# Optimization experiments

Hardware: AMD Instinct MI355X
Metric: run time of the kernel (lower is better)

## Reference

```python
import jax, jax.numpy as jnp
import numpy as np
from jax import lax

N, E, G = 20000, 640000, 16
NA, H, NG, L, NC = 21, 128, 50, 6, 97
CUTOFF = 10.0
LOG2 = 0.6931471805599453

def ssp(v):
    # ShiftedSoftplus: softplus(x) - log(2)
    return jax.nn.softplus(v) - LOG2

def setup_inputs() -> dict:
    key = jax.random.key(0)
    ks = jax.random.split(key, 24)
    s = 0.08  # xavier-ish scale for 128-wide layers
    inp = {
        "x": jax.random.normal(ks[0], (N, NA), dtype=jnp.float32),
        "pos": jax.random.uniform(ks[1], (N, 3), dtype=jnp.float32, minval=0.0, maxval=30.0),
        "edge_index": jax.random.randint(ks[2], (2, E), 0, N, dtype=jnp.int64),
        "batch": jnp.sort(jax.random.randint(ks[3], (N,), 0, G, dtype=jnp.int64)),
        # embedding Linear(21 -> 128), weights stored [in, out]
        "emb_w": jax.random.normal(ks[4], (NA, H), dtype=jnp.float32) * 0.15,
        "emb_b": jnp.zeros((H,), dtype=jnp.float32),
        # per-interaction-block params, stacked over L layers
        "mlp1_w": jax.random.normal(ks[5], (L, NG, H), dtype=jnp.float32) * 0.12,
        "mlp1_b": jnp.zeros((L, H), dtype=jnp.float32),
        "mlp2_w": jax.random.normal(ks[6], (L, H, H), dtype=jnp.float32) * s,
        "mlp2_b": jnp.zeros((L, H), dtype=jnp.float32),
        "conv1_w": jax.random.normal(ks[7], (L, H, H), dtype=jnp.float32) * s,  # no bias
        "conv2_w": jax.random.normal(ks[8], (L, H, H), dtype=jnp.float32) * s,
        "conv2_b": jnp.zeros((L, H), dtype=jnp.float32),
        "lin_w": jax.random.normal(ks[9], (L, H, H), dtype=jnp.float32) * s,
        "lin_b": jnp.zeros((L, H), dtype=jnp.float32),
        # head (note: original reuses self.lin1 twice, act is ReLU, dropout eval=identity)
        "lin1_w": jax.random.normal(ks[10], (H, H), dtype=jnp.float32) * s,
        "lin1_b": jnp.zeros((H,), dtype=jnp.float32),
        "lin2_w": jax.random.normal(ks[11], (H, NC), dtype=jnp.float32) * s,
        "lin2_b": jnp.zeros((NC,), dtype=jnp.float32),
    }
    return inp

def reference(x, pos, edge_index, batch, emb_w, emb_b, mlp1_w, mlp1_b, mlp2_w,
              mlp2_b, conv1_w, conv2_w, conv2_b, lin_w, lin_b, lin1_w, lin1_b,
              lin2_w, lin2_b):
    row, col = edge_index[0], edge_index[1]  # source j, target i
    d = pos[row] - pos[col]                  # [E,3]
    edge_weight = jnp.sqrt(jnp.sum(d * d, axis=-1))  # [E]
    # Gaussian smearing
    offset = jnp.linspace(0.0, CUTOFF, NG)
    coeff = -0.5 / (offset[1] - offset[0]) ** 2
    edge_attr = jnp.exp(coeff * (edge_weight[:, None] - offset[None, :]) ** 2)  # [E,NG]
    # cosine cutoff
    C = 0.5 * (jnp.cos(edge_weight * jnp.pi / CUTOFF) + 1.0)  # [E]

    h = x @ emb_w + emb_b  # [N,H]

    def block(h, p):
        m1w, m1b, m2w, m2b, c1w, c2w, c2b, lw, lb = p
        # edge MLP filter times cutoff envelope
        Wf = (ssp(edge_attr @ m1w + m1b) @ m2w + m2b) * C[:, None]  # [E,H]
        hx = h @ c1w                                 # lin1 (no bias)
        msg = hx[row] * Wf                           # gather + modulate
        agg = jax.ops.segment_sum(msg, col, num_segments=N)  # scatter-add
        y = ssp(agg @ c2w + c2b)
        y = y @ lw + lb
        return h + y, None

    h, _ = lax.scan(block, h, (mlp1_w, mlp1_b, mlp2_w, mlp2_b,
                               conv1_w, conv2_w, conv2_b, lin_w, lin_b))

    h = jax.nn.relu(h @ lin1_w + lin1_b)
    # global mean pool
    ones = jnp.ones((N,), dtype=h.dtype)
    counts = jnp.maximum(jax.ops.segment_sum(ones, batch, num_segments=G), 1.0)
    graph_emb = jax.ops.segment_sum(h, batch, num_segments=G) / counts[:, None]  # [G,H]
    h2 = jax.nn.relu(graph_emb @ lin1_w + lin1_b)  # lin1 reused; dropout=identity (eval)
    out = h2 @ lin2_w + lin2_b                     # [G,NC]
    return graph_emb, out
```

## Files before the change

kernel.cpp:

```cpp
#include <hip/hip_runtime.h>
#include <hip/hip_bf16.h>

#define HD 128
#define NGAUSS 50
#define NLAYER 6
#define NGRAPH 16
#define NCLS 97
#define NTAB2 8192
#define WMAX 12.0f

typedef __attribute__((ext_vector_type(8))) short bf16x8;
typedef __attribute__((ext_vector_type(4))) float f32x4;
typedef __attribute__((ext_vector_type(8))) ushort u16x8;
typedef __attribute__((ext_vector_type(4))) ushort u16x4;

__device__ __forceinline__ float ssp_f(float x) {
    float e = __expf(-fabsf(x));
    return fmaxf(x, 0.0f) + __logf(0.5f + 0.5f * e);
}
__device__ __forceinline__ ushort f2bf(float f) {
    uint u = __float_as_uint(f);
    return (ushort)((u + 0x7FFFu + ((u >> 16) & 1u)) >> 16);
}
__device__ __forceinline__ float bf2f(ushort s) {
    return __uint_as_float(((uint)s) << 16);
}

__global__ void hist_kernel(const int* __restrict__ col, int* __restrict__ deg, int E) {
    int e = blockIdx.x * blockDim.x + threadIdx.x;
    if (e < E) atomicAdd(&deg[col[e]], 1);
}

__global__ void scan1_kernel(const int* __restrict__ deg, int* __restrict__ rowp,
                             int* __restrict__ bsum, int N) {
    __shared__ int sm[256];
    const int t = threadIdx.x, i = blockIdx.x * 256 + t;
    int v = (i < N) ? deg[i] : 0;
    sm[t] = v;
    __syncthreads();
    for (int off = 1; off < 256; off <<= 1) {
        int x = sm[t];
        int a = (t >= off) ? sm[t - off] : 0;
        __syncthreads();
        sm[t] = x + a;
        __syncthreads();
    }
    if (i < N) rowp[i] = sm[t] - v;
    if (t == 255) bsum[blockIdx.x] = sm[255];
}
__global__ void scan2_kernel(const int* __restrict__ bsum, int* __restrict__ boff,
                             int NB, int* __restrict__ rowpN) {
    __shared__ int sm[256];
    const int t = threadIdx.x;
    int v = (t < NB) ? bsum[t] : 0;
    sm[t] = v;
    __syncthreads();
    for (int off = 1; off < 256; off <<= 1) {
        int x = sm[t];
        int a = (t >= off) ? sm[t - off] : 0;
        __syncthreads();
        sm[t] = x + a;
        __syncthreads();
    }
    if (t < NB) boff[t] = sm[t] - v;
    if (t == 255) *rowpN = sm[255];
}
__global__ void scan3_kernel(int* __restrict__ rowp, const int* __restrict__ boff,
                             int* __restrict__ cursor, int N) {
    int i = blockIdx.x * blockDim.x + threadIdx.x;
    if (i < N) {
        int r = rowp[i] + boff[i >> 8];
        rowp[i] = r;
        cursor[i] = r;
    }
}

__global__ void fill_kernel(const int* __restrict__ row, const int* __restrict__ col,
                            const float* __restrict__ pos, int* __restrict__ cursor,
                            uint* __restrict__ meta, int E) {
    int e = blockIdx.x * blockDim.x + threadIdx.x;
    if (e >= E) return;
    int c = col[e], r = row[e];
    int slot = atomicAdd(&cursor[c], 1);
    float dx = pos[r*3+0] - pos[c*3+0];
    float dy = pos[r*3+1] - pos[c*3+1];
    float dz = pos[r*3+2] - pos[c*3+2];
    float w = sqrtf(dx*dx + dy*dy + dz*dz);
    const float invDW = (float)(NTAB2 - 1) / WMAX;
    int i = (int)(w * invDW + 0.5f);
    i = min(i, NTAB2 - 1);
    meta[slot] = ((uint)r) | (((uint)i) << 16);
}

__global__ void prep_kernel(const float* __restrict__ m1w, const float* __restrict__ c1w,
                            const float* __restrict__ c2w, const float* __restrict__ lw,
                            const float* __restrict__ l1w, const float* __restrict__ m2w,
                            ushort* __restrict__ m1T, ushort* __restrict__ nodeThi,
                            ushort* __restrict__ nodeTlo, ushort* __restrict__ m2T) {
    int idx = blockIdx.x * blockDim.x + threadIdx.x;
    const int S1 = 6*128*64, S2 = 19*128*128, S3 = 6*128*128;
    if (idx < S1) {
        int l = idx / 8192, r = idx % 8192, c = r / 64, k = r % 64;
        float v = (k < NGAUSS) ? m1w[(size_t)l*NGAUSS*128 + k*128 + c] : 0.0f;
        m1T[(size_t)l*8192 + c*64 + k] = f2bf(v);
    } else if (idx < S1 + S2) {
        int j = idx - S1;
        int m = j / 16384, r = j % 16384, c = r / 128, k = r % 128;
        const float* src;
        if (m < 6)       src = c1w + (size_t)m*16384;
        else if (m < 12) src = c2w + (size_t)(m-6)*16384;
        else if (m < 18) src = lw  + (size_t)(m-12)*16384;
        else             src = l1w;
        float v = src[k*128 + c];
        ushort hi = f2bf(v);
        nodeThi[(size_t)m*16384 + c*128 + k] = hi;
        nodeTlo[(size_t)m*16384 + c*128 + k] = f2bf(v - bf2f(hi));
    } else if (idx < S1 + S2 + S3) {
        int j = idx - S1 - S2;
        int l = j / 16384, r = j % 16384, c = r / 128, k = r % 128;
        m2T[(size_t)l*16384 + c*128 + k] = f2bf(m2w[(size_t)l*16384 + k*128 + c]);
    }
}

__global__ void embed_kernel(const float* __restrict__ x,
                             const float* __restrict__ emb_w, const float* __restrict__ emb_b,
                             float* __restrict__ h, int N) {
    int idx = blockIdx.x * blockDim.x + threadIdx.x;
    if (idx >= N * HD) return;
    int n = idx >> 7, t = idx & 127;
    float acc = emb_b[t];
    #pragma unroll
    for (int a = 0; a < 21; ++a) acc += x[n*21 + a] * emb_w[a*HD + t];
    h[idx] = acc;
}

__global__ __launch_bounds__(256, 2) void buildtab_kernel(
        const ushort* __restrict__ m1T_all, const ushort* __restrict__ m2T_all,
        const float* __restrict__ m1b_all, const float* __restrict__ m2b_all,
        ushort* __restrict__ Tb6) {
    __shared__ ushort A1[128 * 64];
    __shared__ ushort B1[128 * 64];
    __shared__ ushort U [128 * 128];
    __shared__ float CV[128];
    char* A1b = (char*)A1;
    char* B1b = (char*)B1;
    char* Ub  = (char*)U;
    const int tid  = threadIdx.x;
    const int lane = tid & 63;
    const int wave = tid >> 6;
    const int l15  = lane & 15;
    const int kgrp = (lane >> 4) * 8;
    const int rbase = wave * 32;
    const int NTILES = NTAB2 / 128;
    const int layer = blockIdx.x / NTILES;
    const int mt    = blockIdx.x % NTILES;
    const ushort* m1T = m1T_all + (size_t)layer * 8192;
    const ushort* m2T = m2T_all + (size_t)layer * 16384;
    const float*  m1b = m1b_all + layer * HD;
    const float*  m2b = m2b_all + layer * HD;

    const float step = 10.0f / 49.0f;
    const float coeff = -0.5f / (step * step);
    const float DW = WMAX / (float)(NTAB2 - 1);

    #pragma unroll
    for (int p = 0; p < 4; ++p) {
        int rr = p * 32 + (tid >> 3);
        int k8 = (tid & 7) * 8;
        u16x8 v = *reinterpret_cast<const u16x8*>(&m1T[(size_t)rr * 64 + k8]);
        *reinterpret_cast<u16x8*>(&B1b[rr*128 + ((2*k8) ^ ((rr & 7) << 4))]) = v;
    }
    if (tid < 128) {
        float w = (float)(mt*128 + tid) * DW;
        CV[tid] = 0.5f * (__cosf(w * 0.31415926535897931f) + 1.0f);
    }

    float b1c[8], b2c[8];
    #pragma unroll
    for (int cb = 0; cb < 8; ++cb) { b1c[cb] = m1b[cb*16 + l15]; b2c[cb] = m2b[cb*16 + l15]; }

    #pragma unroll
    for (int p = 0; p < 4; ++p) {
        int rr = p * 32 + (tid >> 3);
        int k8 = (tid & 7) * 8;
        float w = (float)(mt*128 + rr) * DW;
        u16x8 v;
        #pragma unroll
        for (int j = 0; j < 8; ++j) {
            int k = k8 + j;
            float d = w - (float)k * step;
            float g = (k < NGAUSS) ? __expf(coeff * d * d) : 0.0f;
            v[j] = f2bf(g);
        }
        *reinterpret_cast<u16x8*>(&A1b[rr*128 + ((2*k8) ^ ((rr & 7) << 4))]) = v;
    }
    __syncthreads();

    f32x4 acc1[2][8];
    #pragma unroll
    for (int i = 0; i < 2; ++i)
        #pragma unroll
        for (int j = 0; j < 8; ++j) { acc1[i][j].x=0.f; acc1[i][j].y=0.f; acc1[i][j].z=0.f; acc1[i][j].w=0.f; }
    #pragma unroll
    for (int ks = 0; ks < 2; ++ks) {
        int k = ks*32 + kgrp;
        bf16x8 af[2];
        #pragma unroll
        for (int rt = 0; rt < 2; ++rt) {
            int r = rbase + rt*16 + l15;
            af[rt] = *reinterpret_cast<const bf16x8*>(&A1b[r*128 + ((2*k) ^ ((r & 7) << 4))]);
        }
        #pragma unroll
        for (int cb = 0; cb < 8; ++cb) {
            int c = cb*16 + l15;
            bf16x8 bv = *reinterpret_cast<const bf16x8*>(&B1b[c*128 + ((2*k) ^ ((c & 7) << 4))]);
            acc1[0][cb] = __builtin_amdgcn_mfma_f32_16x16x32_bf16(af[0], bv, acc1[0][cb], 0, 0, 0);
            acc1[1][cb] = __builtin_amdgcn_mfma_f32_16x16x32_bf16(af[1], bv, acc1[1][cb], 0, 0, 0);
        }
    }
    #pragma unroll
    for (int rt = 0; rt < 2; ++rt) {
        #pragma unroll
        for (int cb = 0; cb < 8; ++cb) {
            int c = cb*16 + l15;
            #pragma unroll
            for (int i = 0; i < 4; ++i) {
                int rrow = rbase + rt*16 + (lane >> 4)*4 + i;
                ushort us = f2bf(ssp_f(acc1[rt][cb][i] + b1c[cb]));
                *reinterpret_cast<ushort*>(&Ub[rrow*256 + ((2*c) ^ ((rrow & 7) << 4))]) = us;
            }
        }
    }
    __syncthreads();

    f32x4 acc2[2][8];
    #pragma unroll
    for (int i = 0; i < 2; ++i)
        #pragma unroll
        for (int j = 0; j < 8; ++j) { acc2[i][j].x=0.f; acc2[i][j].y=0.f; acc2[i][j].z=0.f; acc2[i][j].w=0.f; }
    #pragma unroll
    for (int kh = 0; kh < 2; ++kh) {
        if (kh) __syncthreads();
        #pragma unroll
        for (int p = 0; p < 4; ++p) {
            int rr = p * 32 + (tid >> 3);
            int kk = (tid & 7) * 8;
            u16x8 v = *reinterpret_cast<const u16x8*>(&m2T[(size_t)rr*128 + kh*64 + kk]);
            *reinterpret_cast<u16x8*>(&A1b[rr*128 + ((2*kk) ^ ((rr & 7) << 4))]) = v;
        }
        __syncthreads();
        #pragma unroll
        for (int ks2 = 0; ks2 < 2; ++ks2) {
            int ku = kh*64 + ks2*32 + kgrp;
            int kb = ks2*32 + kgrp;
            bf16x8 af[2];
            #pragma unroll
            for (int rt = 0; rt < 2; ++rt) {
                int r = rbase + rt*16 + l15;
                af[rt] = *reinterpret_cast<const bf16x8*>(&Ub[r*256 + ((2*ku) ^ ((r & 7) << 4))]);
            }
            #pragma unroll
            for (int cb = 0; cb < 8; ++cb) {
                int c = cb*16 + l15;
                bf16x8 bv = *reinterpret_cast<const bf16x8*>(&A1b[c*128 + ((2*kb) ^ ((c & 7) << 4))]);
                acc2[0][cb] = __builtin_amdgcn_mfma_f32_16x16x32_bf16(af[0], bv, acc2[0][cb], 0, 0, 0);
                acc2[1][cb] = __builtin_amdgcn_mfma_f32_16x16x32_bf16(af[1], bv, acc2[1][cb], 0, 0, 0);
            }
        }
    }
    __syncthreads();

    #pragma unroll
    for (int rt = 0; rt < 2; ++rt) {
        #pragma unroll
        for (int cb = 0; cb < 8; ++cb) {
            int c = cb*16 + l15;
            #pragma unroll
            for (int i = 0; i < 4; ++i) {
                int rrow = rbase + rt*16 + (lane >> 4)*4 + i;
                U[rrow*128 + c] = f2bf((acc2[rt][cb][i] + b2c[cb]) * CV[rrow]);
            }
        }
    }
    __syncthreads();
    #pragma unroll
    for (int p = 0; p < 8; ++p) {
        int idx = p * 256 + tid;
        int rr = idx >> 4;
        int k8 = (idx & 15) * 8;
        u16x8 v = *reinterpret_cast<const u16x8*>(&U[rr*128 + k8]);
        *reinterpret_cast<u16x8*>(&Tb6[((size_t)layer*NTAB2 + mt*128 + rr)*HD + k8]) = v;
    }
}

template<int EPI>
__global__ __launch_bounds__(256) void gemv64_kernel(
        const float* __restrict__ A, const ushort* __restrict__ BThi,
        const ushort* __restrict__ BTlo, const float* __restrict__ bias,
        float* __restrict__ fdst, ushort* __restrict__ bdst, int mtiles) {
    __shared__ ushort Bw[128 * 256];
    __shared__ ushort A_[64 * 128];
    char* Bwb = (char*)Bw;
    char* Ab  = (char*)A_;
    const int tid  = threadIdx.x;
    const int lane = tid & 63;
    const int wave = tid >> 6;
    const int l15  = lane & 15;
    const int kgrp = (lane >> 4) * 8;
    const int rbase = wave * 16;

    #pragma unroll
    for (int p = 0; p < 16; ++p) {
        int idx = p * 256 + tid;
        int c = idx >> 5;
        int k8 = (idx & 31) * 8;
        const ushort* src = (k8 < 128) ? BThi : BTlo;
        u16x8 v = *reinterpret_cast<const u16x8*>(&src[(size_t)c*128 + (k8 & 127)]);
        *reinterpret_cast<u16x8*>(&Bwb[c*512 + ((2*k8) ^ ((c & 7) << 4))]) = v;
    }
    float bt[8];
    if (EPI == 4) {
        #pragma unroll
        for (int cb = 0; cb < 8; ++cb) bt[cb] = bias[cb*16 + l15];
    }
    __syncthreads();

    for (int mt = blockIdx.x; mt < mtiles; mt += gridDim.x) {
        #pragma unroll
        for (int p = 0; p < 8; ++p) {
            int rr = p * 8 + (tid >> 5);
            int k4 = (tid & 31) * 4;
            f32x4 v = *reinterpret_cast<const f32x4*>(&A[(size_t)(mt*64 + rr)*HD + k4]);
            u16x4 b;
            b.x = f2bf(v.x); b.y = f2bf(v.y); b.z = f2bf(v.z); b.w = f2bf(v.w);
            *reinterpret_cast<u16x4*>(&Ab[rr*256 + ((2*k4) ^ ((rr & 7) << 4))]) = b;
        }
        __syncthreads();

        bf16x8 af[4];
        {
            int r = rbase + l15;
            #pragma unroll
            for (int q = 0; q < 4; ++q)
                af[q] = *reinterpret_cast<const bf16x8*>(&Ab[r*256 + ((2*(q*32 + kgrp)) ^ ((r & 7) << 4))]);
        }
        f32x4 acc[8];
        #pragma unroll
        for (int j = 0; j < 8; ++j) { acc[j].x=0.f; acc[j].y=0.f; acc[j].z=0.f; acc[j].w=0.f; }
        #pragma unroll
        for (int ks = 0; ks < 8; ++ks) {
            int kB = ks*32 + kgrp;
            #pragma unroll
            for (int cb = 0; cb < 8; ++cb) {
                int c = cb*16 + l15;
                bf16x8 bv = *reinterpret_cast<const bf16x8*>(&Bwb[c*512 + ((2*kB) ^ ((c & 7) << 4))]);
                acc[cb] = __builtin_amdgcn_mfma_f32_16x16x32_bf16(af[ks & 3], bv, acc[cb], 0, 0, 0);
            }
        }

        #pragma unroll
        for (int cb = 0; cb < 8; ++cb) {
            int c = cb*16 + l15;
            #pragma unroll
            for (int i = 0; i < 4; ++i) {
                int row = mt*64 + rbase + (lane >> 4)*4 + i;
                size_t off = (size_t)row * HD + c;
                if (EPI == 4) fdst[off] = fmaxf(acc[cb][i] + bt[cb], 0.0f);
                else          bdst[off] = f2bf(acc[cb][i]);
            }
        }
        __syncthreads();
    }
}

__global__ __launch_bounds__(512, 1) void nodefused_kernel(
        const ushort* __restrict__ aggb,
        const ushort* __restrict__ c2hi, const ushort* __restrict__ c2lo,
        const float* __restrict__ c2b,
        const ushort* __restrict__ lwhi, const ushort* __restrict__ lwlo,
        const float* __restrict__ lb,
        float* __restrict__ h, int mtiles) {
    __shared__ ushort W1[128 * 256];
    __shared__ ushort W2[128 * 256];
    __shared__ ushort BUF[32 * 128];
    char* W1b = (char*)W1;
    char* W2b = (char*)W2;
    char* Bu  = (char*)BUF;
    const int tid  = threadIdx.x;
    const int lane = tid & 63;
    const int wave = tid >> 6;
    const int l15  = lane & 15;
    const int kgrp = (lane >> 4) * 8;
    const int wr = (wave & 1) * 16;
    const int wc = (wave >> 1) * 2;

    #pragma unroll
    for (int p = 0; p < 8; ++p) {
        int idx = p * 512 + tid;
        int c = idx >> 5;
        int k8 = (idx & 31) * 8;
        const ushort* s1 = (k8 < 128) ? c2hi : c2lo;
        u16x8 v1 = *reinterpret_cast<const u16x8*>(&s1[(size_t)c*128 + (k8 & 127)]);
        *reinterpret_cast<u16x8*>(&W1b[c*512 + ((2*k8) ^ ((c & 7) << 4))]) = v1;
        const ushort* s2 = (k8 < 128) ? lwhi : lwlo;
        u16x8 v2 = *reinterpret_cast<const u16x8*>(&s2[(size_t)c*128 + (k8 & 127)]);
        *reinterpret_cast<u16x8*>(&W2b[c*512 + ((2*k8) ^ ((c & 7) << 4))]) = v2;
    }
    float b1c[2], b2c[2];
    #pragma unroll
    for (int cb = 0; cb < 2; ++cb) {
        int c = (wc + cb)*16 + l15;
        b1c[cb] = c2b[c];
        b2c[cb] = lb[c];
    }
    __syncthreads();

    for (int mt = blockIdx.x; mt < mtiles; mt += gridDim.x) {
        {
            int rr = tid >> 4;
            int k8 = (tid & 15) * 8;
            u16x8 v = *reinterpret_cast<const u16x8*>(&aggb[(size_t)(mt*32 + rr)*HD + k8]);
            *reinterpret_cast<u16x8*>(&Bu[rr*256 + ((2*k8) ^ ((rr & 7) << 4))]) = v;
        }
        float hp[2][4];
        #pragma unroll
        for (int cb = 0; cb < 2; ++cb) {
            int c = (wc + cb)*16 + l15;
            #pragma unroll
            for (int i = 0; i < 4; ++i) {
                int row = mt*32 + wr + (lane >> 4)*4 + i;
                hp[cb][i] = h[(size_t)row * HD + c];
            }
        }
        __syncthreads();

        bf16x8 af[4];
        {
            int r = wr + l15;
            #pragma unroll
            for (int q = 0; q < 4; ++q)
                af[q] = *reinterpret_cast<const bf16x8*>(&Bu[r*256 + ((2*(q*32 + kgrp)) ^ ((r & 7) << 4))]);
        }
        f32x4 acc[2];
        #pragma unroll
        for (int j = 0; j < 2; ++j) { acc[j].x=0.f; acc[j].y=0.f; acc[j].z=0.f; acc[j].w=0.f; }
        #pragma unroll
        for (int ks = 0; ks < 8; ++ks) {
            int kB = ks*32 + kgrp;
            #pragma unroll
            for (int cb = 0; cb < 2; ++cb) {
                int c = (wc + cb)*16 + l15;
                bf16x8 bv = *reinterpret_cast<const bf16x8*>(&W1b[c*512 + ((2*kB) ^ ((c & 7) << 4))]);
                acc[cb] = __builtin_amdgcn_mfma_f32_16x16x32_bf16(af[ks & 3], bv, acc[cb], 0, 0, 0);
            }
        }
        __syncthreads();

        #pragma unroll
        for (int cb = 0; cb < 2; ++cb) {
            int c = (wc + cb)*16 + l15;
            #pragma unroll
            for (int i = 0; i < 4; ++i) {
                int rrow = wr + (lane >> 4)*4 + i;
                ushort us = f2bf(ssp_f(acc[cb][i] + b1c[cb]));
                *reinterpret_cast<ushort*>(&Bu[rrow*256 + ((2*c) ^ ((rrow & 7) << 4))]) = us;
            }
        }
        __syncthreads();

        {
            int r = wr + l15;
            #pragma unroll
            for (int q = 0; q < 4; ++q)
                af[q] = *reinterpret_cast<const bf16x8*>(&Bu[r*256 + ((2*(q*32 + kgrp)) ^ ((r & 7) << 4))]);
        }
        #pragma unroll
        for (int j = 0; j < 2; ++j) { acc[j].x=0.f; acc[j].y=0.f; acc[j].z=0.f; acc[j].w=0.f; }
        #pragma unroll
        for (int ks = 0; ks < 8; ++ks) {
            int kB = ks*32 + kgrp;
            #pragma unroll
            for (int cb = 0; cb < 2; ++cb) {
                int c = (wc + cb)*16 + l15;
                bf16x8 bv = *reinterpret_cast<const bf16x8*>(&W2b[c*512 + ((2*kB) ^ ((c & 7) << 4))]);
                acc[cb] = __builtin_amdgcn_mfma_f32_16x16x32_bf16(af[ks & 3], bv, acc[cb], 0, 0, 0);
            }
        }
        #pragma unroll
        for (int cb = 0; cb < 2; ++cb) {
            int c = (wc + cb)*16 + l15;
            #pragma unroll
            for (int i = 0; i < 4; ++i) {
                int row = mt*32 + wr + (lane >> 4)*4 + i;
                h[(size_t)row * HD + c] = hp[cb][i] + acc[cb][i] + b2c[cb];
            }
        }
        __syncthreads();
    }
}

__global__ __launch_bounds__(256) void gathersum_kernel(
        const ushort* __restrict__ Tb, const uint* __restrict__ meta,
        const int* __restrict__ rowp, const ushort* __restrict__ hxb,
        ushort* __restrict__ aggb, int N) {
    const int lane = threadIdx.x & 63;
    const int n = blockIdx.x * 4 + (threadIdx.x >> 6);
    if (n >= N) return;
    const int c0 = lane * 2;
    const int s0 = rowp[n], s1 = rowp[n + 1];
    float al[4] = {0.f, 0.f, 0.f, 0.f};
    float ah[4] = {0.f, 0.f, 0.f, 0.f};
    int s = s0;
    for (; s + 16 <= s1; s += 16) {
        uint m[16], tv[16], hv[16];
        #pragma unroll
        for (int k = 0; k < 16; ++k) m[k] = meta[s + k];
        #pragma unroll
        for (int k = 0; k < 16; ++k) {
            tv[k] = *reinterpret_cast<const uint*>(&Tb[(size_t)(m[k] >> 16) * HD + c0]);
            hv[k] = *reinterpret_cast<const uint*>(&hxb[(size_t)(m[k] & 0xFFFFu) * HD + c0]);
        }
        #pragma unroll
        for (int k = 0; k < 16; ++k) {
            al[k & 3] += __uint_as_float(tv[k] << 16) * __uint_as_float(hv[k] << 16);
            ah[k & 3] += __uint_as_float(tv[k] & 0xFFFF0000u) * __uint_as_float(hv[k] & 0xFFFF0000u);
        }
    }
    for (; s + 4 <= s1; s += 4) {
        uint m[4], tv[4], hv[4];
        #pragma unroll
        for (int k = 0; k < 4; ++k) m[k] = meta[s + k];
        #pragma unroll
        for (int k = 0; k < 4; ++k) {
            tv[k] = *reinterpret_cast<const uint*>(&Tb[(size_t)(m[k] >> 16) * HD + c0]);
            hv[k] = *reinterpret_cast<const uint*>(&hxb[(size_t)(m[k] & 0xFFFFu) * HD + c0]);
        }
        #pragma unroll
        for (int k = 0; k < 4; ++k) {
            al[k] += __uint_as_float(tv[k] << 16) * __uint_as_float(hv[k] << 16);
            ah[k] += __uint_as_float(tv[k] & 0xFFFF0000u) * __uint_as_float(hv[k] & 0xFFFF0000u);
        }
    }
    for (; s < s1; ++s) {
        uint m0 = meta[s];
        uint tv = *reinterpret_cast<const uint*>(&Tb[(size_t)(m0 >> 16) * HD + c0]);
        uint hv = *reinterpret_cast<const uint*>(&hxb[(size_t)(m0 & 0xFFFFu) * HD + c0]);
        al[0] += __uint_as_float(tv << 16) * __uint_as_float(hv << 16);
        ah[0] += __uint_as_float(tv & 0xFFFF0000u) * __uint_as_float(hv & 0xFFFF0000u);
    }
    float lo = (al[0] + al[1]) + (al[2] + al[3]);
    float hi = (ah[0] + ah[1]) + (ah[2] + ah[3]);
    uint out = ((uint)f2bf(lo)) | (((uint)f2bf(hi)) << 16);
    *reinterpret_cast<uint*>(&aggb[(size_t)n * HD + c0]) = out;
}

__global__ void pool_kernel(const float* __restrict__ h1, const int* __restrict__ batch,
                            float* __restrict__ gsum, float* __restrict__ gcnt, int N) {
    __shared__ float pool[NGRAPH][HD];
    __shared__ float cnt[NGRAPH];
    const int t = threadIdx.x;
    #pragma unroll
    for (int g = 0; g < NGRAPH; ++g) pool[g][t] = 0.0f;
    if (t < NGRAPH) cnt[t] = 0.0f;
    __syncthreads();
    int chunk = (N + gridDim.x - 1) / gridDim.x;
    int n0 = blockIdx.x * chunk, n1 = min(N, n0 + chunk);
    for (int n = n0; n < n1; ++n) {
        int b = batch[n];
        pool[b][t] += h1[(size_t)n * HD + t];
        if (t == 0) cnt[b] += 1.0f;
    }
    __syncthreads();
    #pragma unroll
    for (int g = 0; g < NGRAPH; ++g) atomicAdd(&gsum[g*HD + t], pool[g][t]);
    if (t < NGRAPH) atomicAdd(&gcnt[t], cnt[t]);
}

__global__ void finalize_kernel(const float* __restrict__ gsum, const float* __restrict__ gcnt,
                                const float* __restrict__ l1w, const float* __restrict__ l1b,
                                const float* __restrict__ l2w, const float* __restrict__ l2b,
                                float* __restrict__ d_out) {
    __shared__ float ge[HD];
    __shared__ float h2[HD];
    const int g = blockIdx.x, t = threadIdx.x;
    float cnt = fmaxf(gcnt[g], 1.0f);
    float v = gsum[g*HD + t] / cnt;
    d_out[g*HD + t] = v;
    ge[t] = v;
    __syncthreads();
    float acc = l1b[t];
    #pragma unroll 8
    for (int k = 0; k < HD; ++k) acc += ge[k] * l1w[k*HD + t];
    h2[t] = fmaxf(acc, 0.0f);
    __syncthreads();
    if (t < NCLS) {
        float o = l2b[t];
        #pragma unroll 8
        for (int k = 0; k < HD; ++k) o += h2[k] * l2w[k*NCLS + t];
        d_out[NGRAPH*HD + g*NCLS + t] = o;
    }
}

extern "C" void kernel_launch(void* const* d_in, const int* in_sizes, int n_in,
                              void* d_out, int out_size, void* d_ws, size_t ws_size,
                              hipStream_t stream) {
    const float* x     = (const float*)d_in[0];
    const float* pos   = (const float*)d_in[1];
    const int*   eidx  = (const int*)d_in[2];
    const int*   batch = (const int*)d_in[3];
    const float* emb_w = (const float*)d_in[4];
    const float* emb_b = (const float*)d_in[5];
    const float* m1w   = (const float*)d_in[6];
    const float* m1b   = (const float*)d_in[7];
    const float* m2w   = (const float*)d_in[8];
    const float* m2b   = (const float*)d_in[9];
    const float* c1w   = (const float*)d_in[10];
    const float* c2w   = (const float*)d_in[11];
    const float* c2b   = (const float*)d_in[12];
    const float* lw    = (const float*)d_in[13];
    const float* lb    = (const float*)d_in[14];
    const float* l1w   = (const float*)d_in[15];
    const float* l1b   = (const float*)d_in[16];
    const float* l2w   = (const float*)d_in[17];
    const float* l2b   = (const float*)d_in[18];

    const int N = in_sizes[0] / 21;
    const int E = in_sizes[2] / 2;
    const int* row = eidx;
    const int* col = eidx + E;
    const int NT64 = (N + 63) / 64;
    const int NT32 = (N + 31) / 32;
    const int NB   = (N + 255) / 256;
    const int Npad = NT64 * 64 + 64;

    size_t off = 0;
    char* base = (char*)d_ws;
    auto alloc = [&](size_t bytes) -> void* {
        off = (off + 255) & ~(size_t)255;
        void* p = base + off;
        off += bytes;
        return p;
    };
    int*    deg     = (int*)alloc((size_t)N * 4);
    int*    cursor  = (int*)alloc((size_t)N * 4);
    int*    rowp    = (int*)alloc((size_t)(N + 1) * 4);
    int*    bsum    = (int*)alloc(512 * 4);
    int*    boff    = (int*)alloc(512 * 4);
    uint*   meta    = (uint*)alloc((size_t)E * 4);
    float*  h       = (float*)alloc((size_t)Npad * HD * 4);
    ushort* hxb     = (ushort*)alloc((size_t)Npad * HD * 2);
    ushort* aggb    = (ushort*)alloc((size_t)Npad * HD * 2);
    float*  h1      = (float*)alloc((size_t)Npad * HD * 4);
    ushort* Tb6     = (ushort*)alloc((size_t)6 * NTAB2 * HD * 2);
    ushort* m1T     = (ushort*)alloc((size_t)6 * 128 * 64 * 2);
    ushort* nodeThi = (ushort*)alloc((size_t)19 * 128 * 128 * 2);
    ushort* nodeTlo = (ushort*)alloc((size_t)19 * 128 * 128 * 2);
    ushort* m2T     = (ushort*)alloc((size_t)6 * 128 * 128 * 2);
    float*  gsum    = (float*)alloc((size_t)NGRAPH * HD * 4);
    float*  gcnt    = (float*)alloc((size_t)NGRAPH * 4);

    prep_kernel<<<1792, 256, 0, stream>>>(m1w, c1w, c2w, lw, l1w, m2w,
                                          m1T, nodeThi, nodeTlo, m2T);
    hipMemsetAsync(deg, 0, (size_t)N * 4, stream);
    hist_kernel<<<(E + 255)/256, 256, 0, stream>>>(col, deg, E);
    scan1_kernel<<<NB, 256, 0, stream>>>(deg, rowp, bsum, N);
    scan2_kernel<<<1, 256, 0, stream>>>(bsum, boff, NB, rowp + N);
    scan3_kernel<<<NB, 256, 0, stream>>>(rowp, boff, cursor, N);
    fill_kernel<<<(E + 255)/256, 256, 0, stream>>>(row, col, pos, cursor, meta, E);
    buildtab_kernel<<<6 * (NTAB2/128), 256, 0, stream>>>(m1T, m2T, m1b, m2b, Tb6);
    embed_kernel<<<(N*HD + 255)/256, 256, 0, stream>>>(x, emb_w, emb_b, h, N);

    gemv64_kernel<5><<<NT64, 256, 0, stream>>>(h, nodeThi, nodeTlo, nullptr,
                                               nullptr, hxb, NT64);

    for (int l = 0; l < NLAYER; ++l) {
        const ushort* c2Thi = nodeThi + (size_t)(6 + l) * 16384;
        const ushort* c2Tlo = nodeTlo + (size_t)(6 + l) * 16384;
        const ushort* lThi  = nodeThi + (size_t)(12 + l) * 16384;
        const ushort* lTlo  = nodeTlo + (size_t)(12 + l) * 16384;

        gathersum_kernel<<<(N + 3)/4, 256, 0, stream>>>(
            Tb6 + (size_t)l * NTAB2 * HD, meta, rowp, hxb, aggb, N);

        nodefused_kernel<<<256, 512, 0, stream>>>(
            aggb, c2Thi, c2Tlo, c2b + l*HD, lThi, lTlo, lb + l*HD, h, NT32);

        if (l < NLAYER - 1) {
            gemv64_kernel<5><<<NT64, 256, 0, stream>>>(
                h, nodeThi + (size_t)(l + 1) * 16384, nodeTlo + (size_t)(l + 1) * 16384,
                nullptr, nullptr, hxb, NT64);
        } else {
            gemv64_kernel<4><<<NT64, 256, 0, stream>>>(
                h, nodeThi + (size_t)18 * 16384, nodeTlo + (size_t)18 * 16384,
                l1b, h1, nullptr, NT64);
        }
    }

    hipMemsetAsync(gsum, 0, (size_t)(NGRAPH*HD + NGRAPH) * 4, stream);
    pool_kernel<<<256, HD, 0, stream>>>(h1, batch, gsum, gcnt, N);
    finalize_kernel<<<NGRAPH, HD, 0, stream>>>(gsum, gcnt, l1w, l1b, l2w, l2b,
                                               (float*)d_out);
}
```

Measured before the change: 444.7 us.

## Sort nodes by degree for gather-sum and drop lo-split weights in hx GEMM

Adds a counting sort of nodes by in-degree (descending) so the gather-sum kernel processes nodes of similar degree together. This reduces load imbalance and tail effects from skewed degrees across waves. Separately, the hx projection GEMM now uses only the hi bf16 weight half, halving its K loop and LDS footprint, while the final head GEMM keeps the hi/lo split. Dropping the lo half lowers the precision of the conv1 projection, and the degree sort adds a few small setup kernels.

After: 516.6 us. 1.16x slower.

```diff
diff --git a/kernel.cpp b/kernel.cpp
--- a/kernel.cpp
+++ b/kernel.cpp
@@ -72,6 +72,34 @@
         int r = rowp[i] + boff[i >> 8];
         rowp[i] = r;
         cursor[i] = r;
+    }
+}
+
+__global__ void dhist_kernel(const int* __restrict__ deg, int* __restrict__ dh, int N) {
+    int i = blockIdx.x * blockDim.x + threadIdx.x;
+    if (i < N) atomicAdd(&dh[min(deg[i], 511)], 1);
+}
+__global__ void dscan_kernel(const int* __restrict__ dh, int* __restrict__ dcur) {
+    __shared__ int sm[512];
+    const int t = threadIdx.x;
+    sm[t] = dh[511 - t];
+    __syncthreads();
+    for (int off = 1; off < 512; off <<= 1) {
+        int x = sm[t];
+        int a = (t >= off) ? sm[t - off] : 0;
+        __syncthreads();
+        sm[t] = x + a;
+        __syncthreads();
+    }
+    dcur[511 - t] = sm[t] - dh[511 - t];
+}
+__global__ void dscatter_kernel(const int* __restrict__ deg, int* __restrict__ dcur,
+                                int* __restrict__ nodeord, int N) {
+    int i = blockIdx.x * blockDim.x + threadIdx.x;
+    if (i < N) {
+        int d = min(deg[i], 511);
+        int p = atomicAdd(&dcur[d], 1);
+        nodeord[p] = i;
     }
 }
 
@@ -293,12 +321,14 @@
     }
 }
 
-template<int EPI>
+template<int EPI, bool SPLIT>
 __global__ __launch_bounds__(256) void gemv64_kernel(
         const float* __restrict__ A, const ushort* __restrict__ BThi,
         const ushort* __restrict__ BTlo, const float* __restrict__ bias,
         float* __restrict__ fdst, ushort* __restrict__ bdst, int mtiles) {
-    __shared__ ushort Bw[128 * 256];
+    constexpr int KW   = SPLIT ? 256 : 128;
+    constexpr int BROW = 2 * KW;
+    __shared__ ushort Bw[128 * KW];
     __shared__ ushort A_[64 * 128];
     char* Bwb = (char*)Bw;
     char* Ab  = (char*)A_;
@@ -309,14 +339,25 @@
     const int kgrp = (lane >> 4) * 8;
     const int rbase = wave * 16;
 
-    #pragma unroll
-    for (int p = 0; p < 16; ++p) {
-        int idx = p * 256 + tid;
-        int c = idx >> 5;
-        int k8 = (idx & 31) * 8;
-        const ushort* src = (k8 < 128) ? BThi : BTlo;
-        u16x8 v = *reinterpret_cast<const u16x8*>(&src[(size_t)c*128 + (k8 & 127)]);
-        *reinterpret_cast<u16x8*>(&Bwb[c*512 + ((2*k8) ^ ((c & 7) << 4))]) = v;
+    if (SPLIT) {
+        #pragma unroll
+        for (int p = 0; p < 16; ++p) {
+            int idx = p * 256 + tid;
+            int c = idx >> 5;
+            int k8 = (idx & 31) * 8;
+            const ushort* src = (k8 < 128) ? BThi : BTlo;
+            u16x8 v = *reinterpret_cast<const u16x8*>(&src[(size_t)c*128 + (k8 & 127)]);
+            *reinterpret_cast<u16x8*>(&Bwb[c*BROW + ((2*k8) ^ ((c & 7) << 4))]) = v;
+        }
+    } else {
+        #pragma unroll
+        for (int p = 0; p < 8; ++p) {
+            int idx = p * 256 + tid;
+            int c = idx >> 4;
+            int k8 = (idx & 15) * 8;
+            u16x8 v = *reinterpret_cast<const u16x8*>(&BThi[(size_t)c*128 + k8]);
+            *reinterpret_cast<u16x8*>(&Bwb[c*BROW + ((2*k8) ^ ((c & 7) << 4))]) = v;
+        }
     }
     float bt[8];
     if (EPI == 4) {
@@ -348,12 +389,12 @@
         #pragma unroll
         for (int j = 0; j < 8; ++j) { acc[j].x=0.f; acc[j].y=0.f; acc[j].z=0.f; acc[j].w=0.f; }
         #pragma unroll
-        for (int ks = 0; ks < 8; ++ks) {
+        for (int ks = 0; ks < (SPLIT ? 8 : 4); ++ks) {
             int kB = ks*32 + kgrp;
             #pragma unroll
             for (int cb = 0; cb < 8; ++cb) {
                 int c = cb*16 + l15;
-                bf16x8 bv = *reinterpret_cast<const bf16x8*>(&Bwb[c*512 + ((2*kB) ^ ((c & 7) << 4))]);
+                bf16x8 bv = *reinterpret_cast<const bf16x8*>(&Bwb[c*BROW + ((2*kB) ^ ((c & 7) << 4))]);
                 acc[cb] = __builtin_amdgcn_mfma_f32_16x16x32_bf16(af[ks & 3], bv, acc[cb], 0, 0, 0);
             }
         }
@@ -501,11 +542,12 @@
 
 __global__ __launch_bounds__(256) void gathersum_kernel(
         const ushort* __restrict__ Tb, const uint* __restrict__ meta,
-        const int* __restrict__ rowp, const ushort* __restrict__ hxb,
-        ushort* __restrict__ aggb, int N) {
+        const int* __restrict__ rowp, const int* __restrict__ nodeord,
+        const ushort* __restrict__ hxb, ushort* __restrict__ aggb, int N) {
     const int lane = threadIdx.x & 63;
-    const int n = blockIdx.x * 4 + (threadIdx.x >> 6);
-    if (n >= N) return;
+    const int gid = blockIdx.x * 4 + (threadIdx.x >> 6);
+    if (gid >= N) return;
+    const int n = nodeord[gid];
     const int c0 = lane * 2;
     const int s0 = rowp[n], s1 = rowp[n + 1];
     float al[4] = {0.f, 0.f, 0.f, 0.f};
@@ -646,6 +688,9 @@
     int*    rowp    = (int*)alloc((size_t)(N + 1) * 4);
     int*    bsum    = (int*)alloc(512 * 4);
     int*    boff    = (int*)alloc(512 * 4);
+    int*    dh      = (int*)alloc(512 * 4);
+    int*    dcur    = (int*)alloc(512 * 4);
+    int*    nodeord = (int*)alloc((size_t)N * 4);
     uint*   meta    = (uint*)alloc((size_t)E * 4);
     float*  h       = (float*)alloc((size_t)Npad * HD * 4);
     ushort* hxb     = (ushort*)alloc((size_t)Npad * HD * 2);
@@ -662,16 +707,20 @@
     prep_kernel<<<1792, 256, 0, stream>>>(m1w, c1w, c2w, lw, l1w, m2w,
                                           m1T, nodeThi, nodeTlo, m2T);
     hipMemsetAsync(deg, 0, (size_t)N * 4, stream);
+    hipMemsetAsync(dh, 0, 512 * 4, stream);
     hist_kernel<<<(E + 255)/256, 256, 0, stream>>>(col, deg, E);
     scan1_kernel<<<NB, 256, 0, stream>>>(deg, rowp, bsum, N);
     scan2_kernel<<<1, 256, 0, stream>>>(bsum, boff, NB, rowp + N);
     scan3_kernel<<<NB, 256, 0, stream>>>(rowp, boff, cursor, N);
+    dhist_kernel<<<NB, 256, 0, stream>>>(deg, dh, N);
+    dscan_kernel<<<1, 512, 0, stream>>>(dh, dcur);
+    dscatter_kernel<<<NB, 256, 0, stream>>>(deg, dcur, nodeord, N);
     fill_kernel<<<(E + 255)/256, 256, 0, stream>>>(row, col, pos, cursor, meta, E);
     buildtab_kernel<<<6 * (NTAB2/128), 256, 0, stream>>>(m1T, m2T, m1b, m2b, Tb6);
     embed_kernel<<<(N*HD + 255)/256, 256, 0, stream>>>(x, emb_w, emb_b, h, N);
 
-    gemv64_kernel<5><<<NT64, 256, 0, stream>>>(h, nodeThi, nodeTlo, nullptr,
-                                               nullptr, hxb, NT64);
+    gemv64_kernel<5, false><<<NT64, 256, 0, stream>>>(h, nodeThi, nullptr, nullptr,
+                                                      nullptr, hxb, NT64);
 
     for (int l = 0; l < NLAYER; ++l) {
         const ushort* c2Thi = nodeThi + (size_t)(6 + l) * 16384;
@@ -680,17 +729,17 @@
         const ushort* lTlo  = nodeTlo + (size_t)(12 + l) * 16384;
 
         gathersum_kernel<<<(N + 3)/4, 256, 0, stream>>>(
-            Tb6 + (size_t)l * NTAB2 * HD, meta, rowp, hxb, aggb, N);
+            Tb6 + (size_t)l * NTAB2 * HD, meta, rowp, nodeord, hxb, aggb, N);
 
         nodefused_kernel<<<256, 512, 0, stream>>>(
             aggb, c2Thi, c2Tlo, c2b + l*HD, lThi, lTlo, lb + l*HD, h, NT32);
 
         if (l < NLAYER - 1) {
-            gemv64_kernel<5><<<NT64, 256, 0, stream>>>(
-                h, nodeThi + (size_t)(l + 1) * 16384, nodeTlo + (size_t)(l + 1) * 16384,
+            gemv64_kernel<5, false><<<NT64, 256, 0, stream>>>(
+                h, nodeThi + (size_t)(l + 1) * 16384, nullptr,
                 nullptr, nullptr, hxb, NT64);
         } else {
-            gemv64_kernel<4><<<NT64, 256, 0, stream>>>(
+            gemv64_kernel<4, true><<<NT64, 256, 0, stream>>>(
                 h, nodeThi + (size_t)18 * 16384, nodeTlo + (size_t)18 * 16384,
                 l1b, h1, nullptr, NT64);
         }
```
